# Kernel optimization log

Measured on AMD Instinct MI355X. Metric: run time of the kernel, lower is better.

Reference implementation:

```python
import jax, jax.numpy as jnp
import numpy as np

EPS = 1e-5
STRIDE = 4
NSAMPLE = 8


def _fps(p, m):
    # furthest point sampling on one cloud p:[n,3] -> int32 indices [m]
    d0 = jnp.sum((p - p[0]) ** 2, axis=-1)
    def step(dist, _):
        nxt = jnp.argmax(dist).astype(jnp.int32)
        d = jnp.sum((p - p[nxt]) ** 2, axis=-1)
        return jnp.minimum(dist, d), nxt
    _, idxs = jax.lax.scan(step, d0, None, length=m - 1)
    return jnp.concatenate([jnp.zeros((1,), jnp.int32), idxs])


def _bn(x, gamma, beta):
    # inference-mode BatchNorm1d with running_mean=0, running_var=1
    return gamma * x / jnp.sqrt(1.0 + EPS) + beta


def _transition_down(p, x, W, gamma, beta):
    # p:[B,n,3], x:[B,n,C]  (stride>1 path of TransitionDown)
    B, n, _ = p.shape
    m = n // STRIDE
    pc = jax.lax.stop_gradient(p)
    idx = jax.vmap(_fps, in_axes=(0, None))(pc, m)              # [B,m]
    n_p = jnp.take_along_axis(p, idx[:, :, None], axis=1)       # [B,m,3]
    npc = jax.lax.stop_gradient(n_p)
    # squared distances sampled->all points, [B,m,n] (no [B,m,n,3] temp)
    d2 = (jnp.sum(npc ** 2, -1)[:, :, None]
          + jnp.sum(pc ** 2, -1)[:, None, :]
          - 2.0 * jnp.einsum('bmd,bnd->bmn', npc, pc))
    _, knn = jax.lax.top_k(-d2, NSAMPLE)                        # [B,m,k]
    gp = jax.vmap(lambda pb, kb: pb[kb])(p, knn)                # [B,m,k,3]
    gx = jax.vmap(lambda xb, kb: xb[kb])(x, knn)                # [B,m,k,C]
    rel = gp - n_p[:, :, None, :]                               # use_xyz=True
    feat = jnp.concatenate([rel, gx], axis=-1)                  # [B,m,k,3+C]
    y = jax.nn.relu(_bn(feat @ W, gamma, beta))
    return n_p, jnp.max(y, axis=2)                              # MaxPool1d(k)


def setup_inputs():
    key = jax.random.key(0)
    ks = jax.random.split(key, 16)
    B, n = 8, 8192
    N = B * n
    inp = {
        'p0': jax.random.normal(ks[0], (N, 3), jnp.float32),
        'x0': jax.random.normal(ks[1], (N, 3), jnp.float32),
        'o0': (jnp.arange(1, B + 1) * n).astype(jnp.int32),
    }
    dims_in = [6, 3 + 32, 3 + 64, 3 + 128, 3 + 256]
    dims_out = [32, 64, 128, 256, 512]
    for i in range(5):
        s = 1.0 / np.sqrt(dims_in[i])
        inp[f'W{i+1}'] = jax.random.uniform(ks[2 + i], (dims_in[i], dims_out[i]), jnp.float32, -s, s)
        inp[f'g{i+1}'] = jnp.ones((dims_out[i],), jnp.float32)
        inp[f'b{i+1}'] = jnp.zeros((dims_out[i],), jnp.float32)
    s1 = 1.0 / np.sqrt(512.0)
    inp['Wc1'] = jax.random.uniform(ks[8], (512, 256), jnp.float32, -s1, s1)
    inp['bc1'] = jax.random.uniform(ks[9], (256,), jnp.float32, -s1, s1)
    inp['gcls'] = jnp.ones((256,), jnp.float32)
    inp['bcls'] = jnp.zeros((256,), jnp.float32)
    s2 = 1.0 / np.sqrt(256.0)
    inp['Wc2'] = jax.random.uniform(ks[10], (256, 40), jnp.float32, -s2, s2)
    inp['bc2'] = jax.random.uniform(ks[11], (40,), jnp.float32, -s2, s2)
    return inp


def reference(p0, x0, o0, W1, g1, b1, W2, g2, b2, W3, g3, b3, W4, g4, b4,
              W5, g5, b5, Wc1, bc1, gcls, bcls, Wc2, bc2):
    B = o0.shape[0]
    n = p0.shape[0] // B  # equal-size segments
    p = p0.reshape(B, n, 3)
    x = jnp.concatenate([p0, x0], axis=1).reshape(B, n, 6)  # c=6: cat(xyz, feat)
    # enc1: stride 1 -> relu(bn(linear(x)))
    x = jax.nn.relu(_bn(x @ W1, g1, b1))
    # enc2..enc5: FPS + KNN group + linear/bn/relu + maxpool over neighbors
    p, x = _transition_down(p, x, W2, g2, b2)
    p, x = _transition_down(p, x, W3, g3, b3)
    p, x = _transition_down(p, x, W4, g4, b4)
    p, x = _transition_down(p, x, W5, g5, b5)
    # offset-based segment mean pooling (equal segments -> mean over axis 1)
    pooled = jnp.mean(x, axis=1)                               # [B,512]
    h = jax.nn.relu(_bn(pooled @ Wc1 + bc1, gcls, bcls))       # dropout eval=id
    return h @ Wc2 + bc2                                       # [B,40]
```

## Files before the change

kernel.cpp:

```cpp
#include <hip/hip_runtime.h>
#include <float.h>

#define BNI 0.9999950000374997f

__device__ __forceinline__ float sq3(float x, float y, float z) {
  return __fadd_rn(__fadd_rn(__fmul_rn(x, x), __fmul_rn(y, y)), __fmul_rn(z, z));
}

__device__ __forceinline__ int key_idx(double k) { return ~__double2loint(k); }

template <int CTRL>
__device__ __forceinline__ double dpp_max(double k) {
  union { double d; int i[2]; } u, r;
  u.d = k;
  r.i[0] = __builtin_amdgcn_mov_dpp(u.i[0], CTRL, 0xF, 0xF, true);
  r.i[1] = __builtin_amdgcn_mov_dpp(u.i[1], CTRL, 0xF, 0xF, true);
  return fmax(k, r.d);
}
__device__ __forceinline__ double swz16_max(double k) {
  union { double d; int i[2]; } u, r;
  u.d = k;
  r.i[0] = __builtin_amdgcn_ds_swizzle(u.i[0], 0x401F);
  r.i[1] = __builtin_amdgcn_ds_swizzle(u.i[1], 0x401F);
  return fmax(k, r.d);
}
__device__ __forceinline__ double bperm32_max(double k, int lane) {
  union { double d; int i[2]; } u, r;
  u.d = k;
  int addr = ((lane ^ 32) << 2);
  r.i[0] = __builtin_amdgcn_ds_bpermute(addr, u.i[0]);
  r.i[1] = __builtin_amdgcn_ds_bpermute(addr, u.i[1]);
  return fmax(k, r.d);
}
__device__ __forceinline__ double wave_max_key(double k, int lane) {
  k = dpp_max<0xB1>(k);
  k = dpp_max<0x4E>(k);
  k = dpp_max<0x141>(k);
  k = dpp_max<0x140>(k);
  k = swz16_max(k);
  k = bperm32_max(k, lane);
  return k;
}

__global__ void k_prep(const float* __restrict__ p, float4* __restrict__ P4, int N) {
  int i = blockIdx.x * blockDim.x + threadIdx.x;
  if (i < N) {
    float x = p[3 * i], y = p[3 * i + 1], z = p[3 * i + 2];
    P4[i] = make_float4(x, y, z, sq3(x, y, z));
  }
}

__device__ __forceinline__ unsigned mpart3(unsigned x) {
  return (x & 1u) | ((x & 2u) << 2) | ((x & 4u) << 4);
}
__device__ __forceinline__ int cell_id(float4 v, const float* __restrict__ bb) {
  int cx = min(max((int)((v.x - bb[0]) * bb[3]), 0), 7);
  int cy = min(max((int)((v.y - bb[1]) * bb[4]), 0), 7);
  int cz = min(max((int)((v.z - bb[2]) * bb[5]), 0), 7);
  return (int)((mpart3(cx) << 2) | (mpart3(cy) << 1) | mpart3(cz));
}

__global__ __launch_bounds__(256) void k_bbox(const float4* __restrict__ P, int n,
                                              float* __restrict__ bb) {
  __shared__ float sm[6][4];
  int b = blockIdx.x, tid = threadIdx.x, lane = tid & 63, wid = tid >> 6;
  const float4* Pb = P + (size_t)b * n;
  float lx = FLT_MAX, hx = -FLT_MAX, ly = FLT_MAX, hy = -FLT_MAX, lz = FLT_MAX, hz = -FLT_MAX;
  for (int i = tid; i < n; i += 256) {
    float4 v = Pb[i];
    lx = fminf(lx, v.x); hx = fmaxf(hx, v.x);
    ly = fminf(ly, v.y); hy = fmaxf(hy, v.y);
    lz = fminf(lz, v.z); hz = fmaxf(hz, v.z);
  }
#pragma unroll
  for (int off = 1; off < 64; off <<= 1) {
    lx = fminf(lx, __shfl_xor(lx, off)); hx = fmaxf(hx, __shfl_xor(hx, off));
    ly = fminf(ly, __shfl_xor(ly, off)); hy = fmaxf(hy, __shfl_xor(hy, off));
    lz = fminf(lz, __shfl_xor(lz, off)); hz = fmaxf(hz, __shfl_xor(hz, off));
  }
  if (lane == 0) {
    sm[0][wid] = lx; sm[1][wid] = hx; sm[2][wid] = ly;
    sm[3][wid] = hy; sm[4][wid] = lz; sm[5][wid] = hz;
  }
  __syncthreads();
  if (tid == 0) {
    float LX = fminf(fminf(sm[0][0], sm[0][1]), fminf(sm[0][2], sm[0][3]));
    float HX = fmaxf(fmaxf(sm[1][0], sm[1][1]), fmaxf(sm[1][2], sm[1][3]));
    float LY = fminf(fminf(sm[2][0], sm[2][1]), fminf(sm[2][2], sm[2][3]));
    float HY = fmaxf(fmaxf(sm[3][0], sm[3][1]), fmaxf(sm[3][2], sm[3][3]));
    float LZ = fminf(fminf(sm[4][0], sm[4][1]), fminf(sm[4][2], sm[4][3]));
    float HZ = fmaxf(fmaxf(sm[5][0], sm[5][1]), fmaxf(sm[5][2], sm[5][3]));
    float ex = HX - LX, ey = HY - LY, ez = HZ - LZ;
    float* o = bb + b * 8;
    o[0] = LX; o[1] = LY; o[2] = LZ;
    o[3] = ex > 0.f ? 8.f / ex : 0.f;
    o[4] = ey > 0.f ? 8.f / ey : 0.f;
    o[5] = ez > 0.f ? 8.f / ez : 0.f;
  }
}

__global__ void k_hist(const float4* __restrict__ P, const float* __restrict__ bb,
                       int* __restrict__ hist, int n, int total) {
  int i = blockIdx.x * blockDim.x + threadIdx.x;
  if (i >= total) return;
  int b = i / n;
  int cid = cell_id(P[i], bb + b * 8);
  atomicAdd(&hist[b * 512 + cid], 1);
}

__global__ __launch_bounds__(512) void k_scan(const int* __restrict__ hist,
                                              int* __restrict__ cursor) {
  __shared__ int s[512];
  int b = blockIdx.x, t = threadIdx.x;
  int h = hist[b * 512 + t];
  s[t] = h;
  __syncthreads();
  for (int d = 1; d < 512; d <<= 1) {
    int v = (t >= d) ? s[t - d] : 0;
    __syncthreads();
    s[t] += v;
    __syncthreads();
  }
  cursor[b * 512 + t] = s[t] - h;
}

__global__ void k_scatter(const float4* __restrict__ P, const float* __restrict__ bb,
                          int* __restrict__ cursor, float4* __restrict__ Psort,
                          int n, int total) {
  int i = blockIdx.x * blockDim.x + threadIdx.x;
  if (i >= total) return;
  int b = i / n, il = i - b * n;
  float4 v = P[i];
  int cid = cell_id(v, bb + b * 8);
  int pos = atomicAdd(&cursor[b * 512 + cid], 1);
  Psort[(size_t)b * n + pos] = make_float4(v.x, v.y, v.z, __int_as_float(il));
}

template <int PT, int NW>
__device__ __forceinline__ void fps_body(
    const float4* __restrict__ Psort, const float4* __restrict__ Porig,
    int n, int m, int* __restrict__ out_idx, int b, double* keys ) {
  const int tid = threadIdx.x;
  const int lane = tid & 63, wid = tid >> 6;
  const float4* PS = Psort + (size_t)b * n;
  const float4* PO = Porig + (size_t)b * n;

  float px[PT], py[PT], pz[PT], dist[PT];
  int ni[PT];
  const int base = wid * (64 * PT);
#pragma unroll
  for (int k = 0; k < PT; ++k) {
    float4 v = PS[base + k * 64 + lane];
    px[k] = v.x; py[k] = v.y; pz[k] = v.z;
    ni[k] = ~__float_as_int(v.w);
  }
  float lx = px[0], hx = px[0], ly = py[0], hy = py[0], lz = pz[0], hz = pz[0];
#pragma unroll
  for (int k = 1; k < PT; ++k) {
    lx = fminf(lx, px[k]); hx = fmaxf(hx, px[k]);
    ly = fminf(ly, py[k]); hy = fmaxf(hy, py[k]);
    lz = fminf(lz, pz[k]); hz = fmaxf(hz, pz[k]);
  }
#pragma unroll
  for (int off = 1; off < 64; off <<= 1) {
    lx = fminf(lx, __shfl_xor(lx, off)); hx = fmaxf(hx, __shfl_xor(hx, off));
    ly = fminf(ly, __shfl_xor(ly, off)); hy = fmaxf(hy, __shfl_xor(hy, off));
    lz = fminf(lz, __shfl_xor(lz, off)); hz = fmaxf(hz, __shfl_xor(hz, off));
  }
  if (tid == 0) out_idx[(size_t)b * m] = 0;

  float4 q0 = PO[0];
  double lk = -1.0;
#pragma unroll
  for (int k = 0; k < PT; ++k) {
    float dx = __fsub_rn(px[k], q0.x), dy = __fsub_rn(py[k], q0.y), dz = __fsub_rn(pz[k], q0.z);
    float d = sq3(dx, dy, dz);
    dist[k] = d;
    lk = fmax(lk, __hiloint2double(__float_as_int(d), ni[k]));
  }
  double wkey = wave_max_key(lk, lane);

  for (int t = 1; t < m; ++t) {
    int buf = t & 1;
    if (lane == 0) keys[buf * 16 + wid] = wkey;
    __syncthreads();
    double kb = keys[buf * 16 + (lane & (NW - 1))];
    if (NW >= 2)  kb = dpp_max<0xB1>(kb);
    if (NW >= 4)  kb = dpp_max<0x4E>(kb);
    if (NW >= 8)  kb = dpp_max<0x141>(kb);
    if (NW >= 16) kb = dpp_max<0x140>(kb);
    int wi = key_idx(kb);
    if (tid == 0) out_idx[(size_t)b * m + t] = wi;
    if (t + 1 >= m) break;
    float4 qq = PO[wi];
    float tx = fmaxf(fmaxf(__fsub_rn(lx, qq.x), __fsub_rn(qq.x, hx)), 0.f);
    float ty = fmaxf(fmaxf(__fsub_rn(ly, qq.y), __fsub_rn(qq.y, hy)), 0.f);
    float tz = fmaxf(fmaxf(__fsub_rn(lz, qq.z), __fsub_rn(qq.z, hz)), 0.f);
    float lb = sq3(tx, ty, tz);
    float wv = __uint_as_float((unsigned)__double2hiint(wkey));
    if (lb < wv) {
      double lk2 = -1.0;
#pragma unroll
      for (int k = 0; k < PT; ++k) {
        float dx = __fsub_rn(px[k], qq.x), dy = __fsub_rn(py[k], qq.y), dz = __fsub_rn(pz[k], qq.z);
        float d = sq3(dx, dy, dz);
        float nd = fminf(dist[k], d);
        dist[k] = nd;
        lk2 = fmax(lk2, __hiloint2double(__float_as_int(nd), ni[k]));
      }
      wkey = wave_max_key(lk2, lane);
    }
  }
}

__device__ __forceinline__ void enc1_body(
    const float* __restrict__ p0, const float* __restrict__ x0,
    const float* __restrict__ W, const float* __restrict__ g,
    const float* __restrict__ bt, float* __restrict__ X, int N, int t) {
  int pt = t >> 5, c = t & 31;
  if (pt >= N) return;
  float i0 = p0[pt * 3], i1 = p0[pt * 3 + 1], i2 = p0[pt * 3 + 2];
  float i3 = x0[pt * 3], i4 = x0[pt * 3 + 1], i5 = x0[pt * 3 + 2];
  float a = i0 * W[c] + i1 * W[32 + c] + i2 * W[64 + c] +
            i3 * W[96 + c] + i4 * W[128 + c] + i5 * W[160 + c];
  a = a * (g[c] * BNI) + bt[c];
  X[(size_t)pt * 32 + c] = fmaxf(a, 0.f);
}

__device__ void knn_body(const float4* __restrict__ Pq, const float4* __restrict__ Pc,
                         int n, int m, int* __restrict__ knn, int gw) {
  int lane = threadIdx.x & 63;
  int b = gw / m;
  float4 q = Pq[gw];
  const float4* C = Pc + (size_t)b * n;
  float ad[8];
  int ai[8];
#pragma unroll
  for (int s = 0; s < 8; ++s) { ad[s] = FLT_MAX; ai[s] = 0x7fffffff; }
  for (int j = lane; j < n; j += 64) {
    float4 c = C[j];
    float dot = __fadd_rn(__fadd_rn(__fmul_rn(q.x, c.x), __fmul_rn(q.y, c.y)), __fmul_rn(q.z, c.z));
    float d2 = __fsub_rn(__fadd_rn(q.w, c.w), __fmul_rn(2.f, dot));
    if (d2 < ad[7] || (d2 == ad[7] && j < ai[7])) {
      float cd = d2; int ci = j;
#pragma unroll
      for (int s = 0; s < 8; ++s) {
        bool sw = (cd < ad[s]) || (cd == ad[s] && ci < ai[s]);
        float td = ad[s]; int ti = ai[s];
        ad[s] = sw ? cd : td; ai[s] = sw ? ci : ti;
        cd = sw ? td : cd;  ci = sw ? ti : ci;
      }
    }
  }
  int pos = 0;
  int* kout = knn + (size_t)gw * 8;
#pragma unroll
  for (int r = 0; r < 8; ++r) {
    float hv = FLT_MAX; int hi = 0x7fffffff;
#pragma unroll
    for (int s = 7; s >= 0; --s)
      if (pos == s) { hv = ad[s]; hi = ai[s]; }
    float v = hv; int ix = hi;
#pragma unroll
    for (int off = 1; off < 64; off <<= 1) {
      float ov = __shfl_xor(v, off);
      int oi = __shfl_xor(ix, off);
      if (ov < v || (ov == v && oi < ix)) { v = ov; ix = oi; }
    }
    if (hv == v && hi == ix) pos++;
    if (lane == 0) kout[r] = ix;
  }
}

template <int CINF, int COUT, int NT>
__device__ __forceinline__ void feat_body(
    const float4* __restrict__ Pq, const float4* __restrict__ Pc,
    const float* __restrict__ Xin, const int* __restrict__ knn,
    const float* __restrict__ W, const float* __restrict__ g,
    const float* __restrict__ bt, float* __restrict__ Xout,
    int n, int m, int bi0, int total, char* smem) {
  constexpr int F = 3 + CINF;
  constexpr int NQ = NT / COUT;
  typedef float SF[8][F];
  SF* sf = (SF*)smem;
  int tid = threadIdx.x;
  if (tid < NQ * 8) {
    int ql = tid >> 3, k = tid & 7;
    int bi = bi0 + ql;
    if (bi < total) {
      float4 q = Pq[bi];
      int b = bi / m;
      int nb = knn[(size_t)bi * 8 + k];
      float4 c = Pc[(size_t)b * n + nb];
      sf[ql][k][0] = c.x - q.x;
      sf[ql][k][1] = c.y - q.y;
      sf[ql][k][2] = c.z - q.z;
    }
  }
  for (int e = tid; e < NQ * 8 * CINF; e += NT) {
    int ql = e / (8 * CINF);
    int r = e - ql * (8 * CINF);
    int k = r / CINF, j = r - k * CINF;
    int bi = bi0 + ql;
    if (bi < total) {
      int b = bi / m;
      int nb = knn[(size_t)bi * 8 + k];
      sf[ql][k][3 + j] = Xin[((size_t)b * n + nb) * CINF + j];
    }
  }
  __syncthreads();
  int ql = tid / COUT, c = tid - ql * COUT;
  int bi = bi0 + ql;
  if (bi >= total) return;
  float acc[8] = {0.f, 0.f, 0.f, 0.f, 0.f, 0.f, 0.f, 0.f};
  for (int j = 0; j < F; ++j) {
    float w = W[(size_t)j * COUT + c];
#pragma unroll
    for (int k = 0; k < 8; ++k) acc[k] = fmaf(sf[ql][k][j], w, acc[k]);
  }
  float sc = g[c] * BNI, bb = bt[c];
  float mx = 0.f;
#pragma unroll
  for (int k = 0; k < 8; ++k) mx = fmaxf(mx, fmaf(acc[k], sc, bb));
  Xout[(size_t)bi * COUT + c] = mx;
}

__global__ __launch_bounds__(1024) void k_combo0(
    const float4* __restrict__ Psort, const float4* __restrict__ P2,
    int n, int m2, int* __restrict__ fpsI,
    const float* __restrict__ p0, const float* __restrict__ x0,
    const float* __restrict__ W1, const float* __restrict__ g1,
    const float* __restrict__ b1, float* __restrict__ X1, int N, int B) {
  __shared__ double skeys[32];
  int bid = blockIdx.x;
  if (bid < B) { fps_body<8, 16>(Psort, P2, n, m2, fpsI, bid, skeys); return; }
  enc1_body(p0, x0, W1, g1, b1, X1, N, (bid - B) * 1024 + threadIdx.x);
}

__global__ __launch_bounds__(512) void k_combo1(
    const float4* __restrict__ Psort, const float4* __restrict__ P3,
    int m2, int m3, int* __restrict__ fpsI,
    const float4* __restrict__ P2, int n, int* __restrict__ knnA,
    int B, int totq) {
  __shared__ double skeys[32];
  int bid = blockIdx.x;
  if (bid < B) { fps_body<4, 8>(Psort, P3, m2, m3, fpsI, bid, skeys); return; }
  int gw = (bid - B) * 8 + (threadIdx.x >> 6);
  if (gw < totq) knn_body(P3, P2, n, m2, knnA, gw);
}

__global__ __launch_bounds__(256) void k_combo2(
    const float4* __restrict__ Psort, const float4* __restrict__ P4s,
    int m3, int m4, int* __restrict__ fpsI,
    const float4* __restrict__ P3, int m2, int* __restrict__ knnB,
    const float4* __restrict__ P2, const float* __restrict__ X1,
    const int* __restrict__ knnA,
    const float* __restrict__ W2, const float* __restrict__ g2,
    const float* __restrict__ b2, float* __restrict__ X2,
    int n, int B, int nkb, int totq3, int totq2) {
  __shared__ double skeys[32];
  __shared__ __align__(16) char sfm[4480];
  int bid = blockIdx.x;
  if (bid < B) { fps_body<2, 4>(Psort, P4s, m3, m4, fpsI, bid, skeys); return; }
  bid -= B;
  if (bid < nkb) {
    int gw = bid * 4 + (threadIdx.x >> 6);
    if (gw < totq3) knn_body(P4s, P3, m2, m3, knnB, gw);
    return;
  }
  bid -= nkb;
  feat_body<32, 64, 256>(P3, P2, X1, knnA, W2, g2, b2, X2, n, m2,
                         bid * 4, totq2, sfm);
}

__global__ __launch_bounds__(128) void k_combo3(
    const float4* __restrict__ Psort, const float4* __restrict__ P5,
    int m4, int m5, int* __restrict__ fpsI,
    const float4* __restrict__ P4s, int m3, int* __restrict__ knnA,
    const float4* __restrict__ P3, const float* __restrict__ X2,
    const int* __restrict__ knnB,
    const float* __restrict__ W3, const float* __restrict__ g3,
    const float* __restrict__ b3, float* __restrict__ X3,
    int m2, int B, int nkb, int totq4, int totq3) {
  __shared__ double skeys[32];
  __shared__ __align__(16) char sfm[2144];
  int bid = blockIdx.x;
  if (bid < B) { fps_body<1, 2>(Psort, P5, m4, m5, fpsI, bid, skeys); return; }
  bid -= B;
  if (bid < nkb) {
    int gw = bid * 2 + (threadIdx.x >> 6);
    if (gw < totq4) knn_body(P5, P4s, m3, m4, knnA, gw);
    return;
  }
  bid -= nkb;
  feat_body<64, 128, 128>(P4s, P3, X2, knnB, W3, g3, b3, X3, m2, m3,
                          bid, totq3, sfm);
}

__global__ __launch_bounds__(512) void k_combo4(
    const float4* __restrict__ P6, const float4* __restrict__ P5,
    int m4, int m5, int* __restrict__ knnB,
    const float4* __restrict__ P4s, const float* __restrict__ X3,
    const int* __restrict__ knnA,
    const float* __restrict__ W4, const float* __restrict__ g4,
    const float* __restrict__ b4, float* __restrict__ X4,
    int m3, int nkb, int totq5, int totq4) {
  __shared__ __align__(16) char sfm[8384];
  int bid = blockIdx.x;
  if (bid < nkb) {
    int gw = bid * 8 + (threadIdx.x >> 6);
    if (gw < totq5) knn_body(P6, P5, m4, m5, knnB, gw);
    return;
  }
  bid -= nkb;
  feat_body<128, 256, 512>(P5, P4s, X3, knnA, W4, g4, b4, X4, m3, m4,
                           bid * 2, totq4, sfm);
}

__global__ void k_gather(const float4* __restrict__ Pin, const int* __restrict__ idx,
                         float4* __restrict__ Pout, int n, int m, int total) {
  int t = blockIdx.x * blockDim.x + threadIdx.x;
  if (t >= total) return;
  int b = t / m;
  Pout[t] = Pin[(size_t)b * n + idx[t]];
}

__global__ __launch_bounds__(512) void k_feat5(
    const float4* __restrict__ Pq, const float4* __restrict__ Pc,
    const float* __restrict__ Xin, const int* __restrict__ knn,
    const float* __restrict__ W, const float* __restrict__ g,
    const float* __restrict__ bt, float* __restrict__ Xout, int n, int m) {
  __shared__ __align__(16) char sfm[8 * 259 * 4];
  feat_body<256, 512, 512>(Pq, Pc, Xin, knn, W, g, bt, Xout, n, m,
                           blockIdx.x, gridDim.x, sfm);
}

__global__ __launch_bounds__(512) void k_head(
    const float* __restrict__ X5, const float* __restrict__ Wc1, const float* __restrict__ bc1,
    const float* __restrict__ gc, const float* __restrict__ bcl,
    const float* __restrict__ Wc2, const float* __restrict__ bc2,
    float* __restrict__ out, int m5) {
  __shared__ float sp[512];
  __shared__ float sh[256];
  int b = blockIdx.x, tid = threadIdx.x;
  float s = 0.f;
  for (int i = 0; i < m5; ++i) s += X5[((size_t)b * m5 + i) * 512 + tid];
  sp[tid] = s * (1.0f / m5);
  __syncthreads();
  if (tid < 256) {
    float a = bc1[tid];
    for (int j = 0; j < 512; ++j) a = fmaf(sp[j], Wc1[j * 256 + tid], a);
    a = a * (gc[tid] * BNI) + bcl[tid];
    sh[tid] = fmaxf(a, 0.f);
  }
  __syncthreads();
  if (tid < 40) {
    float a = bc2[tid];
    for (int j = 0; j < 256; ++j) a = fmaf(sh[j], Wc2[j * 40 + tid], a);
    out[b * 40 + tid] = a;
  }
}

extern "C" void kernel_launch(void* const* d_in, const int* in_sizes, int n_in,
                              void* d_out, int out_size, void* d_ws, size_t ws_size,
                              hipStream_t stream) {
  const float* p0 = (const float*)d_in[0];
  const float* x0 = (const float*)d_in[1];
  const int B = in_sizes[2];
  const int N = in_sizes[0] / 3;
  const int n = N / B;
  const float* W1 = (const float*)d_in[3];
  const float* g1 = (const float*)d_in[4];
  const float* b1 = (const float*)d_in[5];
  const float* W2 = (const float*)d_in[6];
  const float* g2 = (const float*)d_in[7];
  const float* b2 = (const float*)d_in[8];
  const float* W3 = (const float*)d_in[9];
  const float* g3 = (const float*)d_in[10];
  const float* b3 = (const float*)d_in[11];
  const float* W4 = (const float*)d_in[12];
  const float* g4 = (const float*)d_in[13];
  const float* b4 = (const float*)d_in[14];
  const float* W5 = (const float*)d_in[15];
  const float* g5 = (const float*)d_in[16];
  const float* b5 = (const float*)d_in[17];
  const float* Wc1 = (const float*)d_in[18];
  const float* bc1 = (const float*)d_in[19];
  const float* gcls = (const float*)d_in[20];
  const float* bcls = (const float*)d_in[21];
  const float* Wc2 = (const float*)d_in[22];
  const float* bc2 = (const float*)d_in[23];
  float* out = (float*)d_out;

  const int m2 = n / 4, m3 = m2 / 4, m4 = m3 / 4, m5 = m4 / 4;

  char* ws = (char*)d_ws;
  size_t off = 0;
  auto alloc = [&](size_t bytes) -> void* {
    void* p = ws + off;
    off += (bytes + 255) & ~(size_t)255;
    return p;
  };
  float4* P2 = (float4*)alloc((size_t)N * 16);
  float* X1 = (float*)alloc((size_t)N * 32 * 4);
  float4* P3 = (float4*)alloc((size_t)B * m2 * 16);
  float4* P4s = (float4*)alloc((size_t)B * m3 * 16);
  float4* P5 = (float4*)alloc((size_t)B * m4 * 16);
  float4* P6 = (float4*)alloc((size_t)B * m5 * 16);
  int* fpsI = (int*)alloc((size_t)B * m2 * 4);
  int* knnA = (int*)alloc((size_t)B * m2 * 8 * 4);
  int* knnB = (int*)alloc((size_t)B * m3 * 8 * 4);
  float* X2 = (float*)alloc((size_t)B * m2 * 64 * 4);
  float* X3 = (float*)alloc((size_t)B * m3 * 128 * 4);
  float* X4 = (float*)alloc((size_t)B * m4 * 256 * 4);
  float* X5 = (float*)alloc((size_t)B * m5 * 512 * 4);
  float4* Psort = (float4*)alloc((size_t)N * 16);
  float* bbox = (float*)alloc((size_t)B * 8 * 4);
  int* hist = (int*)alloc((size_t)B * 512 * 4);
  int* cursor = (int*)alloc((size_t)B * 512 * 4);

  auto sort_stage = [&](const float4* P, int ns) {
    int total = B * ns;
    hipMemsetAsync(hist, 0, (size_t)B * 512 * 4, stream);
    k_bbox<<<B, 256, 0, stream>>>(P, ns, bbox);
    k_hist<<<(total + 255) / 256, 256, 0, stream>>>(P, bbox, hist, ns, total);
    k_scan<<<B, 512, 0, stream>>>(hist, cursor);
    k_scatter<<<(total + 255) / 256, 256, 0, stream>>>(P, bbox, cursor, Psort, ns, total);
  };

  k_prep<<<(N + 255) / 256, 256, 0, stream>>>(p0, P2, N);

  sort_stage(P2, n);
  {
    int eb = (N * 32 + 1023) / 1024;
    k_combo0<<<B + eb, 1024, 0, stream>>>(Psort, P2, n, m2, fpsI,
                                          p0, x0, W1, g1, b1, X1, N, B);
  }
  k_gather<<<(B * m2 + 255) / 256, 256, 0, stream>>>(P2, fpsI, P3, n, m2, B * m2);

  sort_stage(P3, m2);
  {
    int kb = (B * m2 + 7) / 8;
    k_combo1<<<B + kb, 512, 0, stream>>>(Psort, P3, m2, m3, fpsI,
                                         P2, n, knnA, B, B * m2);
  }
  k_gather<<<(B * m3 + 255) / 256, 256, 0, stream>>>(P3, fpsI, P4s, m2, m3, B * m3);

  sort_stage(P4s, m3);
  {
    int nkb = (B * m3 + 3) / 4;
    int fb = (B * m2 + 3) / 4;
    k_combo2<<<B + nkb + fb, 256, 0, stream>>>(
        Psort, P4s, m3, m4, fpsI, P3, m2, knnB, P2, X1, knnA,
        W2, g2, b2, X2, n, B, nkb, B * m3, B * m2);
  }
  k_gather<<<(B * m4 + 255) / 256, 256, 0, stream>>>(P4s, fpsI, P5, m3, m4, B * m4);

  sort_stage(P5, m4);
  {
    int nkb = (B * m4 + 1) / 2;
    int fb = B * m3;
    k_combo3<<<B + nkb + fb, 128, 0, stream>>>(
        Psort, P5, m4, m5, fpsI, P4s, m3, knnA, P3, X2, knnB,
        W3, g3, b3, X3, m2, B, nkb, B * m4, B * m3);
  }
  k_gather<<<(B * m5 + 255) / 256, 256, 0, stream>>>(P5, fpsI, P6, m4, m5, B * m5);

  {
    int nkb = (B * m5 + 7) / 8;
    int fb = (B * m4 + 1) / 2;
    k_combo4<<<nkb + fb, 512, 0, stream>>>(
        P6, P5, m4, m5, knnB, P4s, X3, knnA,
        W4, g4, b4, X4, m3, nkb, B * m5, B * m4);
  }

  k_feat5<<<B * m5, 512, 0, stream>>>(P6, P5, X4, knnB, W5, g5, b5, X5, m4, m5);
  k_head<<<B, 512, 0, stream>>>(X5, Wc1, bc1, gcls, bcls, Wc2, bc2, out, m5);
}
```

Measured before the change: 2.259 ms.

## Cache FPS point coordinates in LDS and use permlane swaps for wave max

Each FPS block now scatters its cloud's coordinates into a shared-memory table indexed by original point id. The per-iteration fetch of the selected point then reads LDS instead of global memory, which sits on the serial critical path. The cross-row wave reduction replaces ds_swizzle and ds_bpermute with permlane16/32 swap builtins, and the per-thread max becomes a tree instead of a linear chain. The price is large static LDS allocations (128 KB for the first combo kernel), which also apply to the non-FPS blocks sharing that kernel and can lower their occupancy.

```diff
diff --git a/kernel.cpp b/kernel.cpp
--- a/kernel.cpp
+++ b/kernel.cpp
@@ -2,6 +2,8 @@
 #include <float.h>
 
 #define BNI 0.9999950000374997f
+
+typedef unsigned int v2u __attribute__((ext_vector_type(2)));
 
 __device__ __forceinline__ float sq3(float x, float y, float z) {
   return __fadd_rn(__fadd_rn(__fmul_rn(x, x), __fmul_rn(y, y)), __fmul_rn(z, z));
@@ -17,28 +19,29 @@
   r.i[1] = __builtin_amdgcn_mov_dpp(u.i[1], CTRL, 0xF, 0xF, true);
   return fmax(k, r.d);
 }
-__device__ __forceinline__ double swz16_max(double k) {
-  union { double d; int i[2]; } u, r;
-  u.d = k;
-  r.i[0] = __builtin_amdgcn_ds_swizzle(u.i[0], 0x401F);
-  r.i[1] = __builtin_amdgcn_ds_swizzle(u.i[1], 0x401F);
-  return fmax(k, r.d);
-}
-__device__ __forceinline__ double bperm32_max(double k, int lane) {
-  union { double d; int i[2]; } u, r;
-  u.d = k;
-  int addr = ((lane ^ 32) << 2);
-  r.i[0] = __builtin_amdgcn_ds_bpermute(addr, u.i[0]);
-  r.i[1] = __builtin_amdgcn_ds_bpermute(addr, u.i[1]);
-  return fmax(k, r.d);
-}
-__device__ __forceinline__ double wave_max_key(double k, int lane) {
+__device__ __forceinline__ double pl16_kmax(double k) {
+  union { double d; unsigned i[2]; } u; u.d = k;
+  v2u a0 = __builtin_amdgcn_permlane16_swap(u.i[0], u.i[0], false, false);
+  v2u a1 = __builtin_amdgcn_permlane16_swap(u.i[1], u.i[1], false, false);
+  k = fmax(k, __hiloint2double((int)a1[0], (int)a0[0]));
+  k = fmax(k, __hiloint2double((int)a1[1], (int)a0[1]));
+  return k;
+}
+__device__ __forceinline__ double pl32_kmax(double k) {
+  union { double d; unsigned i[2]; } u; u.d = k;
+  v2u a0 = __builtin_amdgcn_permlane32_swap(u.i[0], u.i[0], false, false);
+  v2u a1 = __builtin_amdgcn_permlane32_swap(u.i[1], u.i[1], false, false);
+  k = fmax(k, __hiloint2double((int)a1[0], (int)a0[0]));
+  k = fmax(k, __hiloint2double((int)a1[1], (int)a0[1]));
+  return k;
+}
+__device__ __forceinline__ double wave_max_key(double k) {
   k = dpp_max<0xB1>(k);
   k = dpp_max<0x4E>(k);
   k = dpp_max<0x141>(k);
   k = dpp_max<0x140>(k);
-  k = swz16_max(k);
-  k = bperm32_max(k, lane);
+  k = pl16_kmax(k);
+  k = pl32_kmax(k);
   return k;
 }
 
@@ -139,7 +142,8 @@
 template <int PT, int NW>
 __device__ __forceinline__ void fps_body(
     const float4* __restrict__ Psort, const float4* __restrict__ Porig,
-    int n, int m, int* __restrict__ out_idx, int b, double* keys ) {
+    int n, int m, int* __restrict__ out_idx, int b, double* keys ,
+    float4* sQ) {
   const int tid = threadIdx.x;
   const int lane = tid & 63, wid = tid >> 6;
   const float4* PS = Psort + (size_t)b * n;
@@ -152,7 +156,9 @@
   for (int k = 0; k < PT; ++k) {
     float4 v = PS[base + k * 64 + lane];
     px[k] = v.x; py[k] = v.y; pz[k] = v.z;
-    ni[k] = ~__float_as_int(v.w);
+    int oi = __float_as_int(v.w);
+    ni[k] = ~oi;
+    sQ[oi] = make_float4(v.x, v.y, v.z, 0.f);
   }
   float lx = px[0], hx = px[0], ly = py[0], hy = py[0], lz = pz[0], hz = pz[0];
 #pragma unroll
@@ -170,15 +176,18 @@
   if (tid == 0) out_idx[(size_t)b * m] = 0;
 
   float4 q0 = PO[0];
-  double lk = -1.0;
+  double ck[PT];
 #pragma unroll
   for (int k = 0; k < PT; ++k) {
-    float dx = __fsub_rn(px[k], q0.x), dy = __fsub_rn(py[k], q0.y), dz = __fsub_rn(pz[k], q0.z);
-    float d = sq3(dx, dy, dz);
+    float d = sq3(__fsub_rn(px[k], q0.x), __fsub_rn(py[k], q0.y), __fsub_rn(pz[k], q0.z));
     dist[k] = d;
-    lk = fmax(lk, __hiloint2double(__float_as_int(d), ni[k]));
-  }
-  double wkey = wave_max_key(lk, lane);
+    ck[k] = __hiloint2double(__float_as_int(d), ni[k]);
+  }
+#pragma unroll
+  for (int s = 1; s < PT; s <<= 1)
+#pragma unroll
+    for (int k = 0; k + s < PT; k += 2 * s) ck[k] = fmax(ck[k], ck[k + s]);
+  double wkey = wave_max_key(ck[0]);
 
   for (int t = 1; t < m; ++t) {
     int buf = t & 1;
@@ -192,23 +201,26 @@
     int wi = key_idx(kb);
     if (tid == 0) out_idx[(size_t)b * m + t] = wi;
     if (t + 1 >= m) break;
-    float4 qq = PO[wi];
+    float4 qq = sQ[wi];
     float tx = fmaxf(fmaxf(__fsub_rn(lx, qq.x), __fsub_rn(qq.x, hx)), 0.f);
     float ty = fmaxf(fmaxf(__fsub_rn(ly, qq.y), __fsub_rn(qq.y, hy)), 0.f);
     float tz = fmaxf(fmaxf(__fsub_rn(lz, qq.z), __fsub_rn(qq.z, hz)), 0.f);
     float lb = sq3(tx, ty, tz);
     float wv = __uint_as_float((unsigned)__double2hiint(wkey));
     if (lb < wv) {
-      double lk2 = -1.0;
+      double ck2[PT];
 #pragma unroll
       for (int k = 0; k < PT; ++k) {
-        float dx = __fsub_rn(px[k], qq.x), dy = __fsub_rn(py[k], qq.y), dz = __fsub_rn(pz[k], qq.z);
-        float d = sq3(dx, dy, dz);
+        float d = sq3(__fsub_rn(px[k], qq.x), __fsub_rn(py[k], qq.y), __fsub_rn(pz[k], qq.z));
         float nd = fminf(dist[k], d);
         dist[k] = nd;
-        lk2 = fmax(lk2, __hiloint2double(__float_as_int(nd), ni[k]));
+        ck2[k] = __hiloint2double(__float_as_int(nd), ni[k]);
       }
-      wkey = wave_max_key(lk2, lane);
+#pragma unroll
+      for (int s = 1; s < PT; s <<= 1)
+#pragma unroll
+        for (int k = 0; k + s < PT; k += 2 * s) ck2[k] = fmax(ck2[k], ck2[k + s]);
+      wkey = wave_max_key(ck2[0]);
     }
   }
 }
@@ -332,8 +344,9 @@
     const float* __restrict__ W1, const float* __restrict__ g1,
     const float* __restrict__ b1, float* __restrict__ X1, int N, int B) {
   __shared__ double skeys[32];
+  __shared__ float4 sQ[8192];
   int bid = blockIdx.x;
-  if (bid < B) { fps_body<8, 16>(Psort, P2, n, m2, fpsI, bid, skeys); return; }
+  if (bid < B) { fps_body<8, 16>(Psort, P2, n, m2, fpsI, bid, skeys, sQ); return; }
   enc1_body(p0, x0, W1, g1, b1, X1, N, (bid - B) * 1024 + threadIdx.x);
 }
 
@@ -343,8 +356,9 @@
     const float4* __restrict__ P2, int n, int* __restrict__ knnA,
     int B, int totq) {
   __shared__ double skeys[32];
+  __shared__ float4 sQ[2048];
   int bid = blockIdx.x;
-  if (bid < B) { fps_body<4, 8>(Psort, P3, m2, m3, fpsI, bid, skeys); return; }
+  if (bid < B) { fps_body<4, 8>(Psort, P3, m2, m3, fpsI, bid, skeys, sQ); return; }
   int gw = (bid - B) * 8 + (threadIdx.x >> 6);
   if (gw < totq) knn_body(P3, P2, n, m2, knnA, gw);
 }
@@ -359,9 +373,10 @@
     const float* __restrict__ b2, float* __restrict__ X2,
     int n, int B, int nkb, int totq3, int totq2) {
   __shared__ double skeys[32];
+  __shared__ float4 sQ[512];
   __shared__ __align__(16) char sfm[4480];
   int bid = blockIdx.x;
-  if (bid < B) { fps_body<2, 4>(Psort, P4s, m3, m4, fpsI, bid, skeys); return; }
+  if (bid < B) { fps_body<2, 4>(Psort, P4s, m3, m4, fpsI, bid, skeys, sQ); return; }
   bid -= B;
   if (bid < nkb) {
     int gw = bid * 4 + (threadIdx.x >> 6);
@@ -383,9 +398,10 @@
     const float* __restrict__ b3, float* __restrict__ X3,
     int m2, int B, int nkb, int totq4, int totq3) {
   __shared__ double skeys[32];
+  __shared__ float4 sQ[128];
   __shared__ __align__(16) char sfm[2144];
   int bid = blockIdx.x;
-  if (bid < B) { fps_body<1, 2>(Psort, P5, m4, m5, fpsI, bid, skeys); return; }
+  if (bid < B) { fps_body<1, 2>(Psort, P5, m4, m5, fpsI, bid, skeys, sQ); return; }
   bid -= B;
   if (bid < nkb) {
     int gw = bid * 2 + (threadIdx.x >> 6);
```

Result: no change. 2.216 ms (-1.9%).
